# Optimization experiments

Measured on AMD Instinct MI355X. Metric: run time of the kernel, lower is better.

The kernel has to match this reference:

```python
import jax, jax.numpy as jnp
import numpy as np

N = 4096          # number_of_node
DIN = 3           # dim_input (forced: fc1 expects N*dim_input == N*3 after last stage)
DOUT = 4          # dim_output
DACT = N          # dim_action defaults to number_of_node
B = 128


def setup_inputs() -> dict:
    key = jax.random.key(0)
    ks = jax.random.split(key, 12)
    X = jax.random.normal(ks[0], (B, N * DIN), dtype=jnp.float32)
    adj = jax.random.uniform(ks[1], (N, N), dtype=jnp.float32)
    def lin(kw, kb, fan_in, fan_out):
        bound = 1.0 / np.sqrt(fan_in)
        W = jax.random.uniform(kw, (fan_in, fan_out), minval=-bound, maxval=bound, dtype=jnp.float32)
        b = jax.random.uniform(kb, (fan_out,), minval=-bound, maxval=bound, dtype=jnp.float32)
        return W, b
    W1, b1 = lin(ks[2], ks[3], DIN, 4)
    W2, b2 = lin(ks[4], ks[5], 4, DOUT)
    W3, b3 = lin(ks[6], ks[7], DOUT, 3)
    Wfc, bfc = lin(ks[8], ks[9], N * DIN, 54)
    Wout, bout = lin(ks[10], ks[11], 54, DACT)
    return {"X": X, "adj": adj, "W1": W1, "b1": b1, "W2": W2, "b2": b2,
            "W3": W3, "b3": b3, "Wfc": Wfc, "bfc": bfc, "Wout": Wout, "bout": bout}


def reference(X, adj, W1, b1, W2, b2, W3, b3, Wfc, bfc, Wout, bout):
    # X: [B, N*DIN] -> [B, N, DIN]
    h = X.reshape(X.shape[0], N, DIN)
    # three (adj @ h) aggregations fused with tiny Linear + ReLU
    h = jax.nn.relu(jnp.einsum('nm,bmf->bnf', adj, h) @ W1 + b1)   # [B,N,4]
    h = jax.nn.relu(jnp.einsum('nm,bmf->bnf', adj, h) @ W2 + b2)   # [B,N,DOUT]
    h = jax.nn.relu(jnp.einsum('nm,bmf->bnf', adj, h) @ W3 + b3)   # [B,N,3]
    flat = h.reshape(h.shape[0], -1)                               # [B, N*3]
    hid = jax.nn.relu(flat @ Wfc + bfc)                            # [B, 54]
    q_value = hid @ Wout + bout                                    # [B, DACT]
    return q_value
```

## Files before the change

kernel.cpp:

```cpp
#include <hip/hip_runtime.h>


typedef __bf16 bf16x8 __attribute__((ext_vector_type(8)));
typedef float  f32x4  __attribute__((ext_vector_type(4)));

#define N_NODE 4096
#define BATCH  128

__global__ __launch_bounds__(256) void prep_k(const float* __restrict__ adj,
                                              __bf16* __restrict__ adjB,
                                              const float* __restrict__ X,
                                              const float* __restrict__ W1,
                                              __bf16* __restrict__ G0,
                                              float* __restrict__ hid_acc) {
    const int blk = blockIdx.x, tx = threadIdx.x;
    if (blk < 8192) {
        const int g = blk * 256 + tx;
        const int lane = g & 63, ka = (g >> 6) & 127, rb = g >> 13;
        const int row = rb * 16 + (lane & 15);
        const int kb  = ka * 32 + ((lane >> 4) & 3) * 8;
        const float4* s = (const float4*)(adj + (size_t)row * 4096 + kb);
        float4 u = s[0];
        float4 v = s[1];
        bf16x8 o = { (__bf16)u.x, (__bf16)u.y, (__bf16)u.z, (__bf16)u.w,
                     (__bf16)v.x, (__bf16)v.y, (__bf16)v.z, (__bf16)v.w };
        *(bf16x8*)(adjB + (size_t)g * 8) = o;
    } else if (blk < 9216) {
        const int g = (blk - 8192) * 256 + tx;
        const int lp = g & 63, cbg = (g >> 6) & 31, kc = g >> 11;
        const int c = cbg * 16 + (lp & 15);
        const int b = c >> 2, f = c & 3;
        const float w0 = W1[0 * 4 + f], w1 = W1[1 * 4 + f], w2 = W1[2 * 4 + f];
        const int mb = kc * 32 + ((lp >> 4) & 3) * 8;
        const float* Xb = X + (size_t)b * 12288 + (size_t)mb * 3;
        bf16x8 o;
#pragma unroll
        for (int j = 0; j < 8; ++j) {
            const float v = Xb[j * 3 + 0] * w0 + Xb[j * 3 + 1] * w1 + Xb[j * 3 + 2] * w2;
            o[j] = (__bf16)v;
        }
        *(bf16x8*)(G0 + (size_t)g * 8) = o;
    } else {
        const int i = (blk - 9216) * 256 + tx;
        if (i < BATCH * 54) hid_acc[i] = 0.f;
    }
}

template <int MODE>
__global__ __launch_bounds__(1024) void gcn_k(const __bf16* __restrict__ A,
                                              const __bf16* __restrict__ Bp,
                                              const float* __restrict__ Wa,
                                              const float* __restrict__ ba,
                                              const float* __restrict__ Wb,
                                              __bf16* __restrict__ Op,
                                              float* __restrict__ hidOut) {
    __shared__ __align__(16) unsigned char smem[49664];
    const int tx = threadIdx.x;
    const int wave = tx >> 6, lane = tx & 63;
    const int wm = wave >> 3, wk = wave & 7;
    const int quad = lane >> 4, lr = lane & 15;

    const int l = blockIdx.x;
    const int xcd = l & 7, s = l >> 3;
    const int mi = xcd * 4 + (s & 3), ci = s >> 2;
    const int m0 = mi * 128;

    const __bf16* pA[4];
#pragma unroll
    for (int i = 0; i < 4; ++i)
        pA[i] = A + (size_t)(mi * 8 + wm * 4 + i) * 65536 + wk * 512 + lane * 8;
    const __bf16* pB[4];
#pragma unroll
    for (int j = 0; j < 4; ++j)
        pB[j] = Bp + (size_t)(wk * 32 + (ci * 4 + j)) * 512 + lane * 8;

    f32x4 acc[4][4] = {};

#pragma unroll 4
    for (int kt = 0; kt < 16; ++kt) {
        bf16x8 af[4], bv[4];
#pragma unroll
        for (int i = 0; i < 4; ++i)
            af[i] = *(const bf16x8*)(pA[i] + kt * 4096);
#pragma unroll
        for (int j = 0; j < 4; ++j)
            bv[j] = *(const bf16x8*)(pB[j] + kt * 131072);
#pragma unroll
        for (int i = 0; i < 4; ++i)
#pragma unroll
            for (int j = 0; j < 4; ++j)
                acc[i][j] = __builtin_amdgcn_mfma_f32_16x16x32_bf16(
                    af[i], bv[j], acc[i][j], 0, 0, 0);
    }

    float* part = (float*)smem;
    float* Ct   = (float*)(smem + 32768);

    float accf[16];
    if (MODE == 2) {
#pragma unroll
        for (int b = 0; b < 16; ++b) accf[b] = 0.f;
    }

#pragma unroll 1
    for (int h = 0; h < 2; ++h) {
#pragma unroll
        for (int r = 0; r < 4; ++r) {
            __syncthreads();
            if (wm == h) {
#pragma unroll
                for (int u = 0; u < 4; ++u)
                    *(f32x4*)(part + (wk * 4 + u) * 256 + lane * 4) = acc[r][u];
            }
            __syncthreads();
            if (wm == h && wk < 4) {
                f32x4 fin = {};
#pragma unroll
                for (int sl = 0; sl < 8; ++sl)
                    fin += *(const f32x4*)(part + (sl * 4 + wk) * 256 + lane * 4);
#pragma unroll
                for (int rr = 0; rr < 4; ++rr)
                    Ct[(r * 16 + quad * 4 + rr) * 66 + wk * 16 + lr] = fin[rr];
            }
        }
        __syncthreads();

        if (MODE == 0) {
            if (tx < 512) {
                const int lp = tx & 63, cbl = (tx >> 6) & 3, kcl = tx >> 8;
                const int cl = cbl * 16 + (lp & 15);
                const float bf = ba[cl & 3];
                const int mb = kcl * 32 + ((lp >> 4) & 3) * 8;
                bf16x8 o;
#pragma unroll
                for (int j = 0; j < 8; ++j)
                    o[j] = (__bf16)fmaxf(Ct[(mb + j) * 66 + cl] + bf, 0.f);
                *(bf16x8*)(Op + ((size_t)((mi * 4 + h * 2 + kcl) * 32 +
                                          (ci * 4 + cbl)) * 64 + lp) * 8) = o;
            }
        } else if (MODE == 1) {
            if (tx < 512) {
                float W2l[16], W3l[12], bl2[4];
#pragma unroll
                for (int i = 0; i < 16; ++i) W2l[i] = Wa[i];
#pragma unroll
                for (int i = 0; i < 12; ++i) W3l[i] = Wb[i];
#pragma unroll
                for (int i = 0; i < 4; ++i) bl2[i] = ba[i];
                const int lp = tx & 63, cbl = (tx >> 6) & 3, kcl = tx >> 8;
                const int cl = cbl * 16 + (lp & 15);
                const int bloc = cl >> 2, f3 = cl & 3;
                const int mb = kcl * 32 + ((lp >> 4) & 3) * 8;
                bf16x8 o;
#pragma unroll
                for (int j = 0; j < 8; ++j) {
                    const float* row = &Ct[(mb + j) * 66 + bloc * 4];
                    float v = 0.f;
                    if (f3 < 3) {
#pragma unroll
                        for (int fo = 0; fo < 4; ++fo) {
                            const float tmp = fmaxf(row[0] * W2l[fo] + row[1] * W2l[4 + fo] +
                                                    row[2] * W2l[8 + fo] + row[3] * W2l[12 + fo] +
                                                    bl2[fo], 0.f);
                            const float w3a = W3l[fo * 3 + 0], w3b = W3l[fo * 3 + 1],
                                        w3c = W3l[fo * 3 + 2];
                            v += tmp * (f3 == 0 ? w3a : (f3 == 1 ? w3b : w3c));
                        }
                    }
                    o[j] = (__bf16)v;
                }
                *(bf16x8*)(Op + ((size_t)((mi * 4 + h * 2 + kcl) * 32 +
                                          (ci * 4 + cbl)) * 64 + lp) * 8) = o;
            }
        } else {
            const float b30 = ba[0], b31 = ba[1], b32 = ba[2];
            if (lane < 54) {
                for (int nn = 0; nn < 4; ++nn) {
                    const int nl = wave * 4 + nn;
                    const int ng = m0 + h * 64 + nl;
#pragma unroll
                    for (int f = 0; f < 3; ++f) {
                        const float w = Wa[((size_t)ng * 3 + f) * 54 + lane];
                        const float bf = (f == 0) ? b30 : (f == 1 ? b31 : b32);
#pragma unroll
                        for (int b = 0; b < 16; ++b) {
                            const float r = fmaxf(Ct[nl * 66 + b * 4 + f] + bf, 0.f);
                            accf[b] += r * w;
                        }
                    }
                }
            }
        }
    }

    if (MODE == 2) {
        float* red = part;
        __syncthreads();
        if (wave >= 8) {
#pragma unroll
            for (int b = 0; b < 16; ++b)
                red[((wave - 8) * 16 + b) * 64 + lane] = accf[b];
        }
        __syncthreads();
        if (wave < 8) {
#pragma unroll
            for (int b = 0; b < 16; ++b)
                accf[b] += red[(wave * 16 + b) * 64 + lane];
        }
        __syncthreads();
        if (wave < 8) {
#pragma unroll
            for (int b = 0; b < 16; ++b)
                red[(wave * 16 + b) * 64 + lane] = accf[b];
        }
        __syncthreads();
        if (wave == 0 && lane < 54) {
            for (int b = 0; b < 16; ++b) {
                float s2 = 0.f;
#pragma unroll
                for (int w8 = 0; w8 < 8; ++w8)
                    s2 += red[(w8 * 16 + b) * 64 + lane];
                atomicAdd(&hidOut[(ci * 16 + b) * 54 + lane], s2);
            }
        }
    }
}

__global__ __launch_bounds__(256) void fc2_k(const float* __restrict__ hid_acc,
                                             const float* __restrict__ bfc,
                                             const float* __restrict__ Wout,
                                             const float* __restrict__ bout,
                                             float* __restrict__ out) {
    const int tx = threadIdx.x;
    const int a  = blockIdx.x * 256 + tx;
    const int b0 = blockIdx.y * 4;
    __shared__ float hs[4 * 54];
    if (tx < 216) {
        const int j = tx % 54;
        hs[tx] = fmaxf(hid_acc[b0 * 54 + tx] + bfc[j], 0.f);
    }
    __syncthreads();
    float a0 = 0.f, a1 = 0.f, a2 = 0.f, a3 = 0.f;
    for (int j = 0; j < 54; ++j) {
        float w = Wout[(size_t)j * N_NODE + a];
        a0 += hs[0 * 54 + j] * w;
        a1 += hs[1 * 54 + j] * w;
        a2 += hs[2 * 54 + j] * w;
        a3 += hs[3 * 54 + j] * w;
    }
    float bo = bout[a];
    out[(size_t)(b0 + 0) * N_NODE + a] = a0 + bo;
    out[(size_t)(b0 + 1) * N_NODE + a] = a1 + bo;
    out[(size_t)(b0 + 2) * N_NODE + a] = a2 + bo;
    out[(size_t)(b0 + 3) * N_NODE + a] = a3 + bo;
}

extern "C" void kernel_launch(void* const* d_in, const int* in_sizes, int n_in,
                              void* d_out, int out_size, void* d_ws, size_t ws_size,
                              hipStream_t stream) {
    const float* X    = (const float*)d_in[0];
    const float* adj  = (const float*)d_in[1];
    const float* W1   = (const float*)d_in[2];
    const float* b1   = (const float*)d_in[3];
    const float* W2   = (const float*)d_in[4];
    const float* b2   = (const float*)d_in[5];
    const float* W3   = (const float*)d_in[6];
    const float* b3   = (const float*)d_in[7];
    const float* Wfc  = (const float*)d_in[8];
    const float* bfc  = (const float*)d_in[9];
    const float* Wout = (const float*)d_in[10];
    const float* bout = (const float*)d_in[11];
    float* out = (float*)d_out;

    char* w = (char*)d_ws;
    __bf16* adjB = (__bf16*)w;
    __bf16* G0   = (__bf16*)(w + 33554432);
    __bf16* H1   = (__bf16*)(w + 33554432 + 4194304);
    __bf16* H2g  = (__bf16*)(w + 33554432 + 2 * 4194304);
    float*  hid  = (float*)(w + 33554432 + 3 * 4194304);

    prep_k<<<9243, 256, 0, stream>>>(adj, adjB, X, W1, G0, hid);

    gcn_k<0><<<256, 1024, 0, stream>>>(adjB, G0, nullptr, b1, nullptr, H1, nullptr);
    gcn_k<1><<<256, 1024, 0, stream>>>(adjB, H1, W2, b2, W3, H2g, nullptr);
    gcn_k<2><<<256, 1024, 0, stream>>>(adjB, H2g, Wfc, b3, nullptr, nullptr, hid);

    fc2_k<<<dim3(16, 32), 256, 0, stream>>>(hid, bfc, Wout, bout, out);
}
```

Before: 251.0 us.

## Halve gcn block size and split-K width, use tree reduction

The GCN aggregation kernel now runs 512 threads per block (8 waves) instead of 1024, so the split-K factor drops from 8 to 4 and each wave processes twice as many K tiles. The cross-wave partial-sum reduction becomes a two-step pairwise tree in shared memory, replacing the per-row-block loop of eight-way reductions, with fewer barriers. The intent is to cut reduction and synchronisation overhead and improve occupancy via launch bounds (512,4). The trade-off is fewer waves in flight per block to hide memory latency and a longer serial K loop per wave.

```diff
diff --git a/kernel.cpp b/kernel.cpp
--- a/kernel.cpp
+++ b/kernel.cpp
@@ -47,17 +47,17 @@
 }
 
 template <int MODE>
-__global__ __launch_bounds__(1024) void gcn_k(const __bf16* __restrict__ A,
-                                              const __bf16* __restrict__ Bp,
-                                              const float* __restrict__ Wa,
-                                              const float* __restrict__ ba,
-                                              const float* __restrict__ Wb,
-                                              __bf16* __restrict__ Op,
-                                              float* __restrict__ hidOut) {
+__global__ __launch_bounds__(512, 4) void gcn_k(const __bf16* __restrict__ A,
+                                                const __bf16* __restrict__ Bp,
+                                                const float* __restrict__ Wa,
+                                                const float* __restrict__ ba,
+                                                const float* __restrict__ Wb,
+                                                __bf16* __restrict__ Op,
+                                                float* __restrict__ hidOut) {
     __shared__ __align__(16) unsigned char smem[49664];
     const int tx = threadIdx.x;
     const int wave = tx >> 6, lane = tx & 63;
-    const int wm = wave >> 3, wk = wave & 7;
+    const int wm = wave >> 2, wk = wave & 3;
     const int quad = lane >> 4, lr = lane & 15;
 
     const int l = blockIdx.x;
@@ -77,14 +77,14 @@
     f32x4 acc[4][4] = {};
 
 #pragma unroll 4
-    for (int kt = 0; kt < 16; ++kt) {
+    for (int kt = 0; kt < 32; ++kt) {
         bf16x8 af[4], bv[4];
 #pragma unroll
         for (int i = 0; i < 4; ++i)
-            af[i] = *(const bf16x8*)(pA[i] + kt * 4096);
+            af[i] = *(const bf16x8*)(pA[i] + kt * 2048);
 #pragma unroll
         for (int j = 0; j < 4; ++j)
-            bv[j] = *(const bf16x8*)(pB[j] + kt * 131072);
+            bv[j] = *(const bf16x8*)(pB[j] + kt * 65536);
 #pragma unroll
         for (int i = 0; i < 4; ++i)
 #pragma unroll
@@ -104,79 +104,88 @@
 
 #pragma unroll 1
     for (int h = 0; h < 2; ++h) {
-#pragma unroll
-        for (int r = 0; r < 4; ++r) {
-            __syncthreads();
-            if (wm == h) {
-#pragma unroll
-                for (int u = 0; u < 4; ++u)
-                    *(f32x4*)(part + (wk * 4 + u) * 256 + lane * 4) = acc[r][u];
+        __syncthreads();
+        const int sb = (wk >> 1) * 4096;
+        if (wm == h && (wk & 1)) {
+#pragma unroll
+            for (int t = 0; t < 16; ++t)
+                *(f32x4*)(part + sb + t * 256 + lane * 4) = acc[t >> 2][t & 3];
+        }
+        __syncthreads();
+        if (wm == h && !(wk & 1)) {
+#pragma unroll
+            for (int t = 0; t < 16; ++t)
+                acc[t >> 2][t & 3] += *(const f32x4*)(part + sb + t * 256 + lane * 4);
+        }
+        __syncthreads();
+        if (wm == h && wk == 2) {
+#pragma unroll
+            for (int t = 0; t < 16; ++t)
+                *(f32x4*)(part + t * 256 + lane * 4) = acc[t >> 2][t & 3];
+        }
+        __syncthreads();
+        if (wm == h && wk == 0) {
+#pragma unroll
+            for (int t = 0; t < 16; ++t)
+                acc[t >> 2][t & 3] += *(const f32x4*)(part + t * 256 + lane * 4);
+#pragma unroll
+            for (int i = 0; i < 4; ++i)
+#pragma unroll
+                for (int j = 0; j < 4; ++j)
+#pragma unroll
+                    for (int r = 0; r < 4; ++r)
+                        Ct[(i * 16 + quad * 4 + r) * 66 + j * 16 + lr] = acc[i][j][r];
+        }
+        __syncthreads();
+
+        if (MODE == 0) {
+            const int lp = tx & 63, cbl = (tx >> 6) & 3, kcl = tx >> 8;
+            const int cl = cbl * 16 + (lp & 15);
+            const float bf = ba[cl & 3];
+            const int mb = kcl * 32 + ((lp >> 4) & 3) * 8;
+            bf16x8 o;
+#pragma unroll
+            for (int j = 0; j < 8; ++j)
+                o[j] = (__bf16)fmaxf(Ct[(mb + j) * 66 + cl] + bf, 0.f);
+            *(bf16x8*)(Op + ((size_t)((mi * 4 + h * 2 + kcl) * 32 +
+                                      (ci * 4 + cbl)) * 64 + lp) * 8) = o;
+        } else if (MODE == 1) {
+            float W2l[16], W3l[12], bl2[4];
+#pragma unroll
+            for (int i = 0; i < 16; ++i) W2l[i] = Wa[i];
+#pragma unroll
+            for (int i = 0; i < 12; ++i) W3l[i] = Wb[i];
+#pragma unroll
+            for (int i = 0; i < 4; ++i) bl2[i] = ba[i];
+            const int lp = tx & 63, cbl = (tx >> 6) & 3, kcl = tx >> 8;
+            const int cl = cbl * 16 + (lp & 15);
+            const int bloc = cl >> 2, f3 = cl & 3;
+            const int mb = kcl * 32 + ((lp >> 4) & 3) * 8;
+            bf16x8 o;
+#pragma unroll
+            for (int j = 0; j < 8; ++j) {
+                const float* row = &Ct[(mb + j) * 66 + bloc * 4];
+                float v = 0.f;
+                if (f3 < 3) {
+#pragma unroll
+                    for (int fo = 0; fo < 4; ++fo) {
+                        const float tmp = fmaxf(row[0] * W2l[fo] + row[1] * W2l[4 + fo] +
+                                                row[2] * W2l[8 + fo] + row[3] * W2l[12 + fo] +
+                                                bl2[fo], 0.f);
+                        const float w3a = W3l[fo * 3 + 0], w3b = W3l[fo * 3 + 1],
+                                    w3c = W3l[fo * 3 + 2];
+                        v += tmp * (f3 == 0 ? w3a : (f3 == 1 ? w3b : w3c));
+                    }
+                }
+                o[j] = (__bf16)v;
             }
-            __syncthreads();
-            if (wm == h && wk < 4) {
-                f32x4 fin = {};
-#pragma unroll
-                for (int sl = 0; sl < 8; ++sl)
-                    fin += *(const f32x4*)(part + (sl * 4 + wk) * 256 + lane * 4);
-#pragma unroll
-                for (int rr = 0; rr < 4; ++rr)
-                    Ct[(r * 16 + quad * 4 + rr) * 66 + wk * 16 + lr] = fin[rr];
-            }
-        }
-        __syncthreads();
-
-        if (MODE == 0) {
-            if (tx < 512) {
-                const int lp = tx & 63, cbl = (tx >> 6) & 3, kcl = tx >> 8;
-                const int cl = cbl * 16 + (lp & 15);
-                const float bf = ba[cl & 3];
-                const int mb = kcl * 32 + ((lp >> 4) & 3) * 8;
-                bf16x8 o;
-#pragma unroll
-                for (int j = 0; j < 8; ++j)
-                    o[j] = (__bf16)fmaxf(Ct[(mb + j) * 66 + cl] + bf, 0.f);
-                *(bf16x8*)(Op + ((size_t)((mi * 4 + h * 2 + kcl) * 32 +
-                                          (ci * 4 + cbl)) * 64 + lp) * 8) = o;
-            }
-        } else if (MODE == 1) {
-            if (tx < 512) {
-                float W2l[16], W3l[12], bl2[4];
-#pragma unroll
-                for (int i = 0; i < 16; ++i) W2l[i] = Wa[i];
-#pragma unroll
-                for (int i = 0; i < 12; ++i) W3l[i] = Wb[i];
-#pragma unroll
-                for (int i = 0; i < 4; ++i) bl2[i] = ba[i];
-                const int lp = tx & 63, cbl = (tx >> 6) & 3, kcl = tx >> 8;
-                const int cl = cbl * 16 + (lp & 15);
-                const int bloc = cl >> 2, f3 = cl & 3;
-                const int mb = kcl * 32 + ((lp >> 4) & 3) * 8;
-                bf16x8 o;
-#pragma unroll
-                for (int j = 0; j < 8; ++j) {
-                    const float* row = &Ct[(mb + j) * 66 + bloc * 4];
-                    float v = 0.f;
-                    if (f3 < 3) {
-#pragma unroll
-                        for (int fo = 0; fo < 4; ++fo) {
-                            const float tmp = fmaxf(row[0] * W2l[fo] + row[1] * W2l[4 + fo] +
-                                                    row[2] * W2l[8 + fo] + row[3] * W2l[12 + fo] +
-                                                    bl2[fo], 0.f);
-                            const float w3a = W3l[fo * 3 + 0], w3b = W3l[fo * 3 + 1],
-                                        w3c = W3l[fo * 3 + 2];
-                            v += tmp * (f3 == 0 ? w3a : (f3 == 1 ? w3b : w3c));
-                        }
-                    }
-                    o[j] = (__bf16)v;
-                }
-                *(bf16x8*)(Op + ((size_t)((mi * 4 + h * 2 + kcl) * 32 +
-                                          (ci * 4 + cbl)) * 64 + lp) * 8) = o;
-            }
+            *(bf16x8*)(Op + ((size_t)((mi * 4 + h * 2 + kcl) * 32 +
+                                      (ci * 4 + cbl)) * 64 + lp) * 8) = o;
         } else {
             const float b30 = ba[0], b31 = ba[1], b32 = ba[2];
             if (lane < 54) {
-                for (int nn = 0; nn < 4; ++nn) {
-                    const int nl = wave * 4 + nn;
+                for (int nn = 0; nn < 8; ++nn) {
+                    const int nl = wave * 8 + nn;
                     const int ng = m0 + h * 64 + nl;
 #pragma unroll
                     for (int f = 0; f < 3; ++f) {
@@ -196,19 +205,19 @@
     if (MODE == 2) {
         float* red = part;
         __syncthreads();
-        if (wave >= 8) {
+        if (wave >= 4) {
 #pragma unroll
             for (int b = 0; b < 16; ++b)
-                red[((wave - 8) * 16 + b) * 64 + lane] = accf[b];
-        }
-        __syncthreads();
-        if (wave < 8) {
+                red[((wave - 4) * 16 + b) * 64 + lane] = accf[b];
+        }
+        __syncthreads();
+        if (wave < 4) {
 #pragma unroll
             for (int b = 0; b < 16; ++b)
                 accf[b] += red[(wave * 16 + b) * 64 + lane];
         }
         __syncthreads();
-        if (wave < 8) {
+        if (wave < 4) {
 #pragma unroll
             for (int b = 0; b < 16; ++b)
                 red[(wave * 16 + b) * 64 + lane] = accf[b];
@@ -216,10 +225,10 @@
         __syncthreads();
         if (wave == 0 && lane < 54) {
             for (int b = 0; b < 16; ++b) {
-                float s2 = 0.f;
-#pragma unroll
-                for (int w8 = 0; w8 < 8; ++w8)
-                    s2 += red[(w8 * 16 + b) * 64 + lane];
+                const float s2 = red[(0 * 16 + b) * 64 + lane] +
+                                 red[(1 * 16 + b) * 64 + lane] +
+                                 red[(2 * 16 + b) * 64 + lane] +
+                                 red[(3 * 16 + b) * 64 + lane];
                 atomicAdd(&hidOut[(ci * 16 + b) * 54 + lane], s2);
             }
         }
@@ -281,9 +290,9 @@
 
     prep_k<<<9243, 256, 0, stream>>>(adj, adjB, X, W1, G0, hid);
 
-    gcn_k<0><<<256, 1024, 0, stream>>>(adjB, G0, nullptr, b1, nullptr, H1, nullptr);
-    gcn_k<1><<<256, 1024, 0, stream>>>(adjB, H1, W2, b2, W3, H2g, nullptr);
-    gcn_k<2><<<256, 1024, 0, stream>>>(adjB, H2g, Wfc, b3, nullptr, nullptr, hid);
+    gcn_k<0><<<256, 512, 0, stream>>>(adjB, G0, nullptr, b1, nullptr, H1, nullptr);
+    gcn_k<1><<<256, 512, 0, stream>>>(adjB, H1, W2, b2, W3, H2g, nullptr);
+    gcn_k<2><<<256, 512, 0, stream>>>(adjB, H2g, Wfc, b3, nullptr, nullptr, hid);
 
     fc2_k<<<dim3(16, 32), 256, 0, stream>>>(hid, bfc, Wout, bout, out);
 }
```

Result: faster. 244.5 us (-2.6%).
